# Optimization experiments

Measured on AMD Instinct MI355X. Metric: run time of the kernel, lower is better.

Reference implementation:

```python
import jax, jax.numpy as jnp
import numpy as np

N = 20000      # nodes
E = 320000     # edges (before self-loops)
G = 64         # graphs in batch
IN = 128       # input_dim
HID = 64       # hidden_dim
H1 = 4         # heads of conv1
NEG_SLOPE = 0.2


def setup_inputs() -> dict:
    key = jax.random.key(0)
    ks = jax.random.split(key, 14)
    x = jax.random.normal(ks[0], (N, IN), jnp.float32)
    edge_index = jax.random.randint(ks[1], (2, E), 0, N, dtype=jnp.int32)
    batch = jnp.sort(jax.random.randint(ks[2], (N,), 0, G, dtype=jnp.int32))
    # conv1: in=IN, out=HID, heads=4, concat
    W1 = jax.random.normal(ks[3], (IN, H1 * HID), jnp.float32) / np.float32(np.sqrt(IN))
    a_src1 = jax.random.normal(ks[4], (H1, HID), jnp.float32) / np.float32(np.sqrt(HID))
    a_dst1 = jax.random.normal(ks[5], (H1, HID), jnp.float32) / np.float32(np.sqrt(HID))
    b1 = jnp.zeros((H1 * HID,), jnp.float32)
    # conv2: in=4*HID, out=HID, heads=1
    W2 = jax.random.normal(ks[6], (H1 * HID, HID), jnp.float32) / np.float32(np.sqrt(H1 * HID))
    a_src2 = jax.random.normal(ks[7], (1, HID), jnp.float32) / np.float32(np.sqrt(HID))
    a_dst2 = jax.random.normal(ks[8], (1, HID), jnp.float32) / np.float32(np.sqrt(HID))
    b2 = jnp.zeros((HID,), jnp.float32)
    # final linear HID -> 1
    W_lin = jax.random.normal(ks[9], (HID, 1), jnp.float32) / np.float32(np.sqrt(HID))
    b_lin = jnp.zeros((1,), jnp.float32)
    return dict(x=x, edge_index=edge_index, batch=batch,
                W1=W1, a_src1=a_src1, a_dst1=a_dst1, b1=b1,
                W2=W2, a_src2=a_src2, a_dst2=a_dst2, b2=b2,
                W_lin=W_lin, b_lin=b_lin)


def gat_conv(x, src, dst, W, a_src, a_dst, b, heads, out_ch, n_nodes):
    """PyG-style GATConv (v1), concat=True, with self-loops already in src/dst."""
    h = (x @ W).reshape(n_nodes, heads, out_ch)          # [N,H,C]
    s = jnp.einsum('nhc,hc->nh', h, a_src)               # [N,H] per-node src score
    d = jnp.einsum('nhc,hc->nh', h, a_dst)               # [N,H] per-node dst score
    logits = jax.nn.leaky_relu(s[src] + d[dst], NEG_SLOPE)   # [Etot,H]
    # segment softmax over incoming edges of each destination node
    m = jax.ops.segment_max(logits, dst, num_segments=n_nodes)
    m = jnp.where(jnp.isfinite(m), m, 0.0)
    e = jnp.exp(logits - m[dst])                         # [Etot,H]
    denom = jax.ops.segment_sum(e, dst, num_segments=n_nodes)
    alpha = e / denom[dst]                               # every node has a self-loop -> denom>0
    out = jax.ops.segment_sum(alpha[:, :, None] * h[src], dst, num_segments=n_nodes)  # [N,H,C]
    return out.reshape(n_nodes, heads * out_ch) + b


def reference(x, edge_index, batch,
              W1, a_src1, a_dst1, b1,
              W2, a_src2, a_dst2, b2,
              W_lin, b_lin):
    n = x.shape[0]
    loop = jnp.arange(n, dtype=edge_index.dtype)
    src = jnp.concatenate([edge_index[0], loop])   # add self-loops (PyG default)
    dst = jnp.concatenate([edge_index[1], loop])
    h = jax.nn.elu(gat_conv(x, src, dst, W1, a_src1, a_dst1, b1, H1, HID, n))
    h = jax.nn.elu(gat_conv(h, src, dst, W2, a_src2, a_dst2, b2, 1, HID, n))
    # global mean pool over graphs
    sums = jax.ops.segment_sum(h, batch, num_segments=G)                 # [G,HID]
    cnt = jax.ops.segment_sum(jnp.ones((n,), h.dtype), batch, num_segments=G)
    pooled = sums / jnp.maximum(cnt, 1.0)[:, None]
    return (pooled @ W_lin + b_lin).squeeze(-1)    # [G]
```

## Files before the change

kernel.cpp:

```cpp
#include <hip/hip_runtime.h>
#include <hip/hip_bf16.h>
#include <cstdint>


__device__ __forceinline__ float leaky02(float x) { return x > 0.f ? x : 0.2f * x; }
__device__ __forceinline__ float eluf(float x) { return x > 0.f ? x : expm1f(x); }
__device__ __forceinline__ float bf2f(unsigned short u) {
    return __uint_as_float((unsigned)u << 16);
}
__device__ __forceinline__ unsigned short f2bf(float f) {
    unsigned x = __float_as_uint(f);
    return (unsigned short)((x + 0x7FFF + ((x >> 16) & 1)) >> 16);
}
__device__ __forceinline__ float4 cv4(ushort4 u) {
    return make_float4(bf2f(u.x), bf2f(u.y), bf2f(u.z), bf2f(u.w));
}

template <int H>
__device__ __forceinline__ void sgemm_scores_body(
    const float* __restrict__ A, const float* __restrict__ B,
    unsigned short* __restrict__ C, int M, int K,
    const float* __restrict__ asrc, const float* __restrict__ adst,
    float* __restrict__ sT, float* __restrict__ dS, float* __restrict__ wself,
    int bx, int by, float* As_, float* Bs_) {
    constexpr int Nc = H * 64;
    float (*As)[68] = (float(*)[68])As_;
    float (*Bs)[68] = (float(*)[68])Bs_;
    const int tid = threadIdx.x;
    const int bm = bx * 64, bn = by * 64;
    const int ty = tid >> 4, tx = tid & 15;
    float acc[4][4] = {};
    for (int k0 = 0; k0 < K; k0 += 32) {
#pragma unroll
        for (int i = 0; i < 8; i++) {
            int idx = tid + i * 256;
            int m = idx >> 5, kk = idx & 31;
            int gm = bm + m;
            if (gm >= M) gm = 0;
            As[kk][m] = A[(size_t)gm * K + k0 + kk];
        }
#pragma unroll
        for (int i = 0; i < 8; i++) {
            int idx = tid + i * 256;
            int kk = idx >> 6, n = idx & 63;
            Bs[kk][n] = B[(size_t)(k0 + kk) * Nc + bn + n];
        }
        __syncthreads();
#pragma unroll
        for (int kk = 0; kk < 32; kk++) {
            float4 a4 = *(const float4*)&As[kk][ty * 4];
            float4 b4 = *(const float4*)&Bs[kk][tx * 4];
            float av[4] = {a4.x, a4.y, a4.z, a4.w};
            float bv[4] = {b4.x, b4.y, b4.z, b4.w};
#pragma unroll
            for (int r = 0; r < 4; r++)
#pragma unroll
                for (int c2 = 0; c2 < 4; c2++) acc[r][c2] += av[r] * bv[c2];
        }
        __syncthreads();
    }
    const int h = by;
    float sr[4], dr[4];
#pragma unroll
    for (int r = 0; r < 4; r++) {
        float s = 0.f, d = 0.f;
#pragma unroll
        for (int c2 = 0; c2 < 4; c2++) {
            float hv = acc[r][c2];
            s += hv * asrc[h * 64 + tx * 4 + c2];
            d += hv * adst[h * 64 + tx * 4 + c2];
        }
        sr[r] = s;
        dr[r] = d;
    }
#pragma unroll
    for (int off = 1; off <= 8; off <<= 1) {
#pragma unroll
        for (int r = 0; r < 4; r++) {
            sr[r] += __shfl_xor(sr[r], off);
            dr[r] += __shfl_xor(dr[r], off);
        }
    }
#pragma unroll
    for (int r = 0; r < 4; r++) {
        int gm = bm + ty * 4 + r;
        if (gm < M) {
            ushort4 o;
            o.x = f2bf(acc[r][0]);
            o.y = f2bf(acc[r][1]);
            o.z = f2bf(acc[r][2]);
            o.w = f2bf(acc[r][3]);
            *(ushort4*)&C[(size_t)gm * Nc + bn + tx * 4] = o;
            if (tx == 0) {
                sT[(size_t)h * M + gm] = sr[r];
                dS[gm * H + h] = dr[r];
                wself[gm * H + h] = __expf(leaky02(sr[r] + dr[r]));
            }
        }
    }
}

__global__ __launch_bounds__(256) void fused_sgemm4_init_kernel(
    const float* __restrict__ A, const float* __restrict__ B,
    unsigned short* __restrict__ C, int M, int K,
    const float* __restrict__ asrc, const float* __restrict__ adst,
    float* __restrict__ sT, float* __restrict__ dS, float* __restrict__ wself,
    int GBX, int GB1, int4* __restrict__ initp, int colN4, int totN4) {
    __shared__ __align__(16) float As_[32][68];
    __shared__ __align__(16) float Bs_[32][68];
    const int b = blockIdx.x;
    if (b >= GB1) {
        int i = (b - GB1) * 256 + threadIdx.x;
        if (i < totN4)
            initp[i] = (i < colN4) ? make_int4(-1, -1, -1, -1) : make_int4(0, 0, 0, 0);
        return;
    }
    sgemm_scores_body<4>(A, B, C, M, K, asrc, adst, sT, dS, wself,
                         b % GBX, b / GBX, &As_[0][0], &Bs_[0][0]);
}

__global__ __launch_bounds__(256) void sgemm_scores1_kernel(
    const float* __restrict__ A, const float* __restrict__ B,
    unsigned short* __restrict__ C, int M, int K,
    const float* __restrict__ asrc, const float* __restrict__ adst,
    float* __restrict__ sT, float* __restrict__ dS, float* __restrict__ wself) {
    __shared__ __align__(16) float As_[32][68];
    __shared__ __align__(16) float Bs_[32][68];
    sgemm_scores_body<1>(A, B, C, M, K, asrc, adst, sT, dS, wself,
                         blockIdx.x, 0, &As_[0][0], &Bs_[0][0]);
}

__global__ void fill_kernel(const int* __restrict__ src, const int* __restrict__ dst,
                            int* __restrict__ cursor, int* __restrict__ col, int E) {
    int e = blockIdx.x * blockDim.x + threadIdx.x;
    if (e >= E) return;
    int d = dst[e];
    int p = atomicAdd(&cursor[d], 1);
    if (p < 64) col[(d << 6) + p] = src[e];
}

__global__ __launch_bounds__(256) void gat_agg4_kernel(
    const unsigned short* __restrict__ h1, const float* __restrict__ sT,
    const float* __restrict__ dsc, const float* __restrict__ wself,
    const int* __restrict__ cursor, const int* __restrict__ col,
    const float* __restrict__ bias, float* __restrict__ out, int N) {
    const int slice = blockIdx.x & 3;
    const int sub = (blockIdx.x >> 2) & 1;
    const int vgrp = (blockIdx.x >> 3) * 2 + sub;
    const int lane = threadIdx.x & 63;
    const int cq = lane & 15;
    const int vidx = vgrp * 16 + (threadIdx.x >> 6) * 4 + (lane >> 4);
    const bool valid = vidx < N;
    const int v = min(vidx, N - 1);
    const int deg = min(cursor[v], 64);
    const int base = v << 6;
    const int ch = slice * 64 + cq * 4;
    const float* __restrict__ sTh = sT + (size_t)slice * N;
    const unsigned short* __restrict__ hp = h1 + slice * 64 + cq * 4;
    const float dvh = dsc[v * 4 + slice];
    float ws = wself[v * 4 + slice];
    float den = ws;
    float4 hv = cv4(*(const ushort4*)(hp + ((size_t)v << 8)));
    float4 acc = make_float4(ws * hv.x, ws * hv.y, ws * hv.z, ws * hv.w);
    const int end4 = (deg + 3) & ~3;
    int4 c4 = *(const int4*)&col[base];
    for (int j = 0; j < end4; j += 4) {
        int4 cc = c4;
        c4 = *(const int4*)&col[base + j + 4];
        unsigned i0 = (unsigned)max(cc.x, 0), i1 = (unsigned)max(cc.y, 0);
        unsigned i2 = (unsigned)max(cc.z, 0), i3 = (unsigned)max(cc.w, 0);
        float4 h0 = cv4(*(const ushort4*)(hp + ((size_t)i0 << 8)));
        float4 h1v = cv4(*(const ushort4*)(hp + ((size_t)i1 << 8)));
        float4 h2v = cv4(*(const ushort4*)(hp + ((size_t)i2 << 8)));
        float4 h3v = cv4(*(const ushort4*)(hp + ((size_t)i3 << 8)));
        float w0 = (cc.x >= 0) ? __expf(leaky02(sTh[i0] + dvh)) : 0.f;
        float w1 = (cc.y >= 0) ? __expf(leaky02(sTh[i1] + dvh)) : 0.f;
        float w2 = (cc.z >= 0) ? __expf(leaky02(sTh[i2] + dvh)) : 0.f;
        float w3 = (cc.w >= 0) ? __expf(leaky02(sTh[i3] + dvh)) : 0.f;
        den += w0 + w1 + w2 + w3;
        acc.x += w0 * h0.x + w1 * h1v.x + w2 * h2v.x + w3 * h3v.x;
        acc.y += w0 * h0.y + w1 * h1v.y + w2 * h2v.y + w3 * h3v.y;
        acc.z += w0 * h0.z + w1 * h1v.z + w2 * h2v.z + w3 * h3v.z;
        acc.w += w0 * h0.w + w1 * h1v.w + w2 * h2v.w + w3 * h3v.w;
    }
    if (valid) {
        float4 b4 = *(const float4*)&bias[ch];
        float inv = 1.f / den;
        float4 r;
        r.x = eluf(acc.x * inv + b4.x);
        r.y = eluf(acc.y * inv + b4.y);
        r.z = eluf(acc.z * inv + b4.z);
        r.w = eluf(acc.w * inv + b4.w);
        *(float4*)&out[(size_t)v * 256 + ch] = r;
    }
}

__global__ __launch_bounds__(256) void gat_agg1_kernel(
    const unsigned short* __restrict__ h2, const float* __restrict__ sT,
    const float* __restrict__ dsc, const float* __restrict__ wself,
    const int* __restrict__ cursor, const int* __restrict__ col,
    const float* __restrict__ bias, const float* __restrict__ Wlin,
    float* __restrict__ pn, int N) {
    const int lane = threadIdx.x & 63;
    const int cq = lane & 15;
    const int vidx = blockIdx.x * 16 + (threadIdx.x >> 6) * 4 + (lane >> 4);
    const bool valid = vidx < N;
    const int v = min(vidx, N - 1);
    const int deg = min(cursor[v], 64);
    const int base = v << 6;
    const unsigned short* __restrict__ hp = h2 + cq * 4;
    const float dv = dsc[v];
    float ws = wself[v];
    float den = ws;
    float4 hv = cv4(*(const ushort4*)(hp + ((size_t)v << 6)));
    float4 acc = make_float4(ws * hv.x, ws * hv.y, ws * hv.z, ws * hv.w);
    const int end4 = (deg + 3) & ~3;
    int4 c4 = *(const int4*)&col[base];
    for (int j = 0; j < end4; j += 4) {
        int4 cc = c4;
        c4 = *(const int4*)&col[base + j + 4];
        unsigned i0 = (unsigned)max(cc.x, 0), i1 = (unsigned)max(cc.y, 0);
        unsigned i2 = (unsigned)max(cc.z, 0), i3 = (unsigned)max(cc.w, 0);
        float4 h0 = cv4(*(const ushort4*)(hp + ((size_t)i0 << 6)));
        float4 h1v = cv4(*(const ushort4*)(hp + ((size_t)i1 << 6)));
        float4 h2v = cv4(*(const ushort4*)(hp + ((size_t)i2 << 6)));
        float4 h3v = cv4(*(const ushort4*)(hp + ((size_t)i3 << 6)));
        float w0 = (cc.x >= 0) ? __expf(leaky02(sT[i0] + dv)) : 0.f;
        float w1 = (cc.y >= 0) ? __expf(leaky02(sT[i1] + dv)) : 0.f;
        float w2 = (cc.z >= 0) ? __expf(leaky02(sT[i2] + dv)) : 0.f;
        float w3 = (cc.w >= 0) ? __expf(leaky02(sT[i3] + dv)) : 0.f;
        den += w0 + w1 + w2 + w3;
        acc.x += w0 * h0.x + w1 * h1v.x + w2 * h2v.x + w3 * h3v.x;
        acc.y += w0 * h0.y + w1 * h1v.y + w2 * h2v.y + w3 * h3v.y;
        acc.z += w0 * h0.z + w1 * h1v.z + w2 * h2v.z + w3 * h3v.z;
        acc.w += w0 * h0.w + w1 * h1v.w + w2 * h2v.w + w3 * h3v.w;
    }
    float4 b4 = *(const float4*)&bias[cq * 4];
    float4 wl = *(const float4*)&Wlin[cq * 4];
    float inv = 1.f / den;
    float p = eluf(acc.x * inv + b4.x) * wl.x + eluf(acc.y * inv + b4.y) * wl.y +
              eluf(acc.z * inv + b4.z) * wl.z + eluf(acc.w * inv + b4.w) * wl.w;
    p += __shfl_xor(p, 1);
    p += __shfl_xor(p, 2);
    p += __shfl_xor(p, 4);
    p += __shfl_xor(p, 8);
    if (valid && cq == 0) pn[v] = p;
}

__global__ __launch_bounds__(64) void finalize_kernel(const float* __restrict__ pn,
                                                      const int* __restrict__ batch,
                                                      const float* __restrict__ blin,
                                                      float* __restrict__ outp, int N, int G) {
    const int g = blockIdx.x;
    const int lane = threadIdx.x;
    int lo = 0, hi = N;
    while (lo < hi) { int mid = (lo + hi) >> 1; if (batch[mid] < g) lo = mid + 1; else hi = mid; }
    int lo2 = lo, hi2 = N;
    while (lo2 < hi2) { int mid = (lo2 + hi2) >> 1; if (batch[mid] < g + 1) lo2 = mid + 1; else hi2 = mid; }
    float s = 0.f;
    for (int i = lo + lane; i < hi2; i += 64) s += pn[i];
#pragma unroll
    for (int off = 32; off > 0; off >>= 1) s += __shfl_xor(s, off);
    if (lane == 0) {
        float cnt = (float)(hi2 - lo);
        outp[g] = s / fmaxf(cnt, 1.f) + blin[0];
    }
}

extern "C" void kernel_launch(void* const* d_in, const int* in_sizes, int n_in,
                              void* d_out, int out_size, void* d_ws, size_t ws_size,
                              hipStream_t stream) {
    const float* x      = (const float*)d_in[0];
    const int*   ei     = (const int*)d_in[1];
    const int*   batch  = (const int*)d_in[2];
    const float* W1     = (const float*)d_in[3];
    const float* a_src1 = (const float*)d_in[4];
    const float* a_dst1 = (const float*)d_in[5];
    const float* b1     = (const float*)d_in[6];
    const float* W2     = (const float*)d_in[7];
    const float* a_src2 = (const float*)d_in[8];
    const float* a_dst2 = (const float*)d_in[9];
    const float* b2     = (const float*)d_in[10];
    const float* Wlin   = (const float*)d_in[11];
    const float* blin   = (const float*)d_in[12];

    const int N = in_sizes[2];
    const int E = in_sizes[1] / 2;
    const int G = out_size;
    const int* src = ei;
    const int* dst = ei + E;

    char* ws = (char*)d_ws;
    size_t off = 0;
    auto carve = [&](size_t bytes) -> char* {
        char* p = ws + off;
        off = (off + bytes + 255) & ~(size_t)255;
        return p;
    };
    unsigned short* h1 = (unsigned short*)carve((size_t)N * 256 * 2);
    float* out1    = (float*)carve((size_t)N * 256 * 4);
    unsigned short* h2 = (unsigned short*)carve((size_t)N * 64 * 2);
    float* sT1     = (float*)carve((size_t)4 * N * 4);
    float* d1      = (float*)carve((size_t)N * 4 * 4);
    float* wself1  = (float*)carve((size_t)N * 4 * 4);
    float* sT2     = (float*)carve((size_t)N * 4);
    float* d2      = (float*)carve((size_t)N * 4);
    float* wself2  = (float*)carve((size_t)N * 4);
    int*   colcur  = (int*)carve(((size_t)N * 64 + N) * 4);
    float* pn      = (float*)carve((size_t)N * 4);
    int* col = colcur;
    int* cursor = colcur + (size_t)N * 64;

    const int GBX = (N + 63) / 64;
    const int GB1 = GBX * 4;
    const int totN4 = (N * 64 + N) / 4;
    const int colN4 = N * 16;
    const int GBI = (totN4 + 255) / 256;

    fused_sgemm4_init_kernel<<<GB1 + GBI, 256, 0, stream>>>(
        x, W1, h1, N, 128, a_src1, a_dst1, sT1, d1, wself1,
        GBX, GB1, (int4*)colcur, colN4, totN4);
    fill_kernel<<<(E + 255) / 256, 256, 0, stream>>>(src, dst, cursor, col, E);

    const int nodeGroups32 = (N + 31) / 32;
    gat_agg4_kernel<<<8 * nodeGroups32, 256, 0, stream>>>(h1, sT1, d1, wself1, cursor, col,
                                                          b1, out1, N);
    sgemm_scores1_kernel<<<dim3(GBX, 1), 256, 0, stream>>>(
        out1, W2, h2, N, 256, a_src2, a_dst2, sT2, d2, wself2);
    gat_agg1_kernel<<<(N + 15) / 16, 256, 0, stream>>>(h2, sT2, d2, wself2, cursor, col,
                                                       b2, Wlin, pn, N);
    finalize_kernel<<<G, 64, 0, stream>>>(pn, batch, blin, (float*)d_out, N, G);
}
```

Baseline: 125.3 us.

## Store layer-1 output in bf16, fuse CSR fill into GEMM, fold finalize into last block

The layer-1 aggregation output is now written in bf16 and the second GEMM reads it as bf16, which halves that intermediate's traffic. The CSR fill moves into the layer-1 GEMM launch, and a separate init kernel clears the buffers first. The mean-pool finalize runs inside the last block of the layer-2 aggregation, found with an atomic done counter. This removes a launch but adds bf16 rounding of the layer-2 input, and the finalize work now sits on a single block.

Result: slower. 214.7 us (+71.4%).

```diff
diff --git a/kernel.cpp b/kernel.cpp
--- a/kernel.cpp
+++ b/kernel.cpp
@@ -15,10 +15,18 @@
 __device__ __forceinline__ float4 cv4(ushort4 u) {
     return make_float4(bf2f(u.x), bf2f(u.y), bf2f(u.z), bf2f(u.w));
 }
-
-template <int H>
+__device__ __forceinline__ float ldA(const float* p) { return *p; }
+__device__ __forceinline__ float ldA(const unsigned short* p) { return bf2f(*p); }
+
+__global__ void init_kernel(int4* __restrict__ p, int colN4, int totN4) {
+    int i = blockIdx.x * blockDim.x + threadIdx.x;
+    if (i < totN4)
+        p[i] = (i < colN4) ? make_int4(-1, -1, -1, -1) : make_int4(0, 0, 0, 0);
+}
+
+template <int H, typename AT>
 __device__ __forceinline__ void sgemm_scores_body(
-    const float* __restrict__ A, const float* __restrict__ B,
+    const AT* __restrict__ A, const float* __restrict__ B,
     unsigned short* __restrict__ C, int M, int K,
     const float* __restrict__ asrc, const float* __restrict__ adst,
     float* __restrict__ sT, float* __restrict__ dS, float* __restrict__ wself,
@@ -37,7 +45,7 @@
             int m = idx >> 5, kk = idx & 31;
             int gm = bm + m;
             if (gm >= M) gm = 0;
-            As[kk][m] = A[(size_t)gm * K + k0 + kk];
+            As[kk][m] = ldA(&A[(size_t)gm * K + k0 + kk]);
         }
 #pragma unroll
         for (int i = 0; i < 8; i++) {
@@ -100,50 +108,45 @@
     }
 }
 
-__global__ __launch_bounds__(256) void fused_sgemm4_init_kernel(
+__global__ __launch_bounds__(256) void fused_sgemm4_fill_kernel(
     const float* __restrict__ A, const float* __restrict__ B,
     unsigned short* __restrict__ C, int M, int K,
     const float* __restrict__ asrc, const float* __restrict__ adst,
     float* __restrict__ sT, float* __restrict__ dS, float* __restrict__ wself,
-    int GBX, int GB1, int4* __restrict__ initp, int colN4, int totN4) {
+    int GBX, int GB1, const int* __restrict__ src, const int* __restrict__ dst,
+    int* __restrict__ cursor, int* __restrict__ col, int E) {
     __shared__ __align__(16) float As_[32][68];
     __shared__ __align__(16) float Bs_[32][68];
     const int b = blockIdx.x;
     if (b >= GB1) {
-        int i = (b - GB1) * 256 + threadIdx.x;
-        if (i < totN4)
-            initp[i] = (i < colN4) ? make_int4(-1, -1, -1, -1) : make_int4(0, 0, 0, 0);
+        int e = (b - GB1) * 256 + threadIdx.x;
+        if (e < E) {
+            int d = dst[e];
+            int p = atomicAdd(&cursor[d], 1);
+            if (p < 64) col[(d << 6) + p] = src[e];
+        }
         return;
     }
-    sgemm_scores_body<4>(A, B, C, M, K, asrc, adst, sT, dS, wself,
-                         b % GBX, b / GBX, &As_[0][0], &Bs_[0][0]);
+    sgemm_scores_body<4, float>(A, B, C, M, K, asrc, adst, sT, dS, wself,
+                                b % GBX, b / GBX, &As_[0][0], &Bs_[0][0]);
 }
 
 __global__ __launch_bounds__(256) void sgemm_scores1_kernel(
-    const float* __restrict__ A, const float* __restrict__ B,
+    const unsigned short* __restrict__ A, const float* __restrict__ B,
     unsigned short* __restrict__ C, int M, int K,
     const float* __restrict__ asrc, const float* __restrict__ adst,
     float* __restrict__ sT, float* __restrict__ dS, float* __restrict__ wself) {
     __shared__ __align__(16) float As_[32][68];
     __shared__ __align__(16) float Bs_[32][68];
-    sgemm_scores_body<1>(A, B, C, M, K, asrc, adst, sT, dS, wself,
-                         blockIdx.x, 0, &As_[0][0], &Bs_[0][0]);
-}
-
-__global__ void fill_kernel(const int* __restrict__ src, const int* __restrict__ dst,
-                            int* __restrict__ cursor, int* __restrict__ col, int E) {
-    int e = blockIdx.x * blockDim.x + threadIdx.x;
-    if (e >= E) return;
-    int d = dst[e];
-    int p = atomicAdd(&cursor[d], 1);
-    if (p < 64) col[(d << 6) + p] = src[e];
+    sgemm_scores_body<1, unsigned short>(A, B, C, M, K, asrc, adst, sT, dS, wself,
+                                         blockIdx.x, 0, &As_[0][0], &Bs_[0][0]);
 }
 
 __global__ __launch_bounds__(256) void gat_agg4_kernel(
     const unsigned short* __restrict__ h1, const float* __restrict__ sT,
     const float* __restrict__ dsc, const float* __restrict__ wself,
     const int* __restrict__ cursor, const int* __restrict__ col,
-    const float* __restrict__ bias, float* __restrict__ out, int N) {
+    const float* __restrict__ bias, unsigned short* __restrict__ out, int N) {
     const int slice = blockIdx.x & 3;
     const int sub = (blockIdx.x >> 2) & 1;
     const int vgrp = (blockIdx.x >> 3) * 2 + sub;
@@ -158,10 +161,10 @@
     const float* __restrict__ sTh = sT + (size_t)slice * N;
     const unsigned short* __restrict__ hp = h1 + slice * 64 + cq * 4;
     const float dvh = dsc[v * 4 + slice];
-    float ws = wself[v * 4 + slice];
-    float den = ws;
+    float wsf = wself[v * 4 + slice];
+    float den = wsf;
     float4 hv = cv4(*(const ushort4*)(hp + ((size_t)v << 8)));
-    float4 acc = make_float4(ws * hv.x, ws * hv.y, ws * hv.z, ws * hv.w);
+    float4 acc = make_float4(wsf * hv.x, wsf * hv.y, wsf * hv.z, wsf * hv.w);
     const int end4 = (deg + 3) & ~3;
     int4 c4 = *(const int4*)&col[base];
     for (int j = 0; j < end4; j += 4) {
@@ -186,21 +189,23 @@
     if (valid) {
         float4 b4 = *(const float4*)&bias[ch];
         float inv = 1.f / den;
-        float4 r;
-        r.x = eluf(acc.x * inv + b4.x);
-        r.y = eluf(acc.y * inv + b4.y);
-        r.z = eluf(acc.z * inv + b4.z);
-        r.w = eluf(acc.w * inv + b4.w);
-        *(float4*)&out[(size_t)v * 256 + ch] = r;
-    }
-}
-
-__global__ __launch_bounds__(256) void gat_agg1_kernel(
+        ushort4 o;
+        o.x = f2bf(eluf(acc.x * inv + b4.x));
+        o.y = f2bf(eluf(acc.y * inv + b4.y));
+        o.z = f2bf(eluf(acc.z * inv + b4.z));
+        o.w = f2bf(eluf(acc.w * inv + b4.w));
+        *(ushort4*)&out[(size_t)v * 256 + ch] = o;
+    }
+}
+
+__global__ __launch_bounds__(256) void gat_agg1_fin_kernel(
     const unsigned short* __restrict__ h2, const float* __restrict__ sT,
     const float* __restrict__ dsc, const float* __restrict__ wself,
     const int* __restrict__ cursor, const int* __restrict__ col,
     const float* __restrict__ bias, const float* __restrict__ Wlin,
-    float* __restrict__ pn, int N) {
+    float* __restrict__ pn, const int* __restrict__ batch,
+    const float* __restrict__ blin, float* __restrict__ outp,
+    int* __restrict__ done, int N, int G) {
     const int lane = threadIdx.x & 63;
     const int cq = lane & 15;
     const int vidx = blockIdx.x * 16 + (threadIdx.x >> 6) * 4 + (lane >> 4);
@@ -210,10 +215,10 @@
     const int base = v << 6;
     const unsigned short* __restrict__ hp = h2 + cq * 4;
     const float dv = dsc[v];
-    float ws = wself[v];
-    float den = ws;
+    float wsf = wself[v];
+    float den = wsf;
     float4 hv = cv4(*(const ushort4*)(hp + ((size_t)v << 6)));
-    float4 acc = make_float4(ws * hv.x, ws * hv.y, ws * hv.z, ws * hv.w);
+    float4 acc = make_float4(wsf * hv.x, wsf * hv.y, wsf * hv.z, wsf * hv.w);
     const int end4 = (deg + 3) & ~3;
     int4 c4 = *(const int4*)&col[base];
     for (int j = 0; j < end4; j += 4) {
@@ -245,25 +250,30 @@
     p += __shfl_xor(p, 4);
     p += __shfl_xor(p, 8);
     if (valid && cq == 0) pn[v] = p;
-}
-
-__global__ __launch_bounds__(64) void finalize_kernel(const float* __restrict__ pn,
-                                                      const int* __restrict__ batch,
-                                                      const float* __restrict__ blin,
-                                                      float* __restrict__ outp, int N, int G) {
-    const int g = blockIdx.x;
-    const int lane = threadIdx.x;
-    int lo = 0, hi = N;
-    while (lo < hi) { int mid = (lo + hi) >> 1; if (batch[mid] < g) lo = mid + 1; else hi = mid; }
-    int lo2 = lo, hi2 = N;
-    while (lo2 < hi2) { int mid = (lo2 + hi2) >> 1; if (batch[mid] < g + 1) lo2 = mid + 1; else hi2 = mid; }
-    float s = 0.f;
-    for (int i = lo + lane; i < hi2; i += 64) s += pn[i];
-#pragma unroll
-    for (int off = 32; off > 0; off >>= 1) s += __shfl_xor(s, off);
-    if (lane == 0) {
-        float cnt = (float)(hi2 - lo);
-        outp[g] = s / fmaxf(cnt, 1.f) + blin[0];
+
+    __shared__ int lastFlag;
+    __threadfence();
+    if (threadIdx.x == 0) {
+        int old = atomicAdd(done, 1);
+        lastFlag = (old == (int)gridDim.x - 1) ? 1 : 0;
+    }
+    __syncthreads();
+    if (!lastFlag) return;
+    __threadfence();
+    const int g = threadIdx.x >> 2, sub = threadIdx.x & 3;
+    if (g < G) {
+        int lo = 0, hi = N;
+        while (lo < hi) { int mid = (lo + hi) >> 1; if (batch[mid] < g) lo = mid + 1; else hi = mid; }
+        int lo2 = lo, hi2 = N;
+        while (lo2 < hi2) { int mid = (lo2 + hi2) >> 1; if (batch[mid] < g + 1) lo2 = mid + 1; else hi2 = mid; }
+        float s = 0.f;
+        for (int i = lo + sub; i < hi2; i += 4) s += pn[i];
+        s += __shfl_xor(s, 1);
+        s += __shfl_xor(s, 2);
+        if (sub == 0) {
+            float cnt = (float)(hi2 - lo);
+            outp[g] = s / fmaxf(cnt, 1.f) + blin[0];
+        }
     }
 }
 
@@ -297,37 +307,37 @@
         off = (off + bytes + 255) & ~(size_t)255;
         return p;
     };
-    unsigned short* h1 = (unsigned short*)carve((size_t)N * 256 * 2);
-    float* out1    = (float*)carve((size_t)N * 256 * 4);
-    unsigned short* h2 = (unsigned short*)carve((size_t)N * 64 * 2);
+    unsigned short* h1   = (unsigned short*)carve((size_t)N * 256 * 2);
+    unsigned short* out1 = (unsigned short*)carve((size_t)N * 256 * 2);
+    unsigned short* h2   = (unsigned short*)carve((size_t)N * 64 * 2);
     float* sT1     = (float*)carve((size_t)4 * N * 4);
     float* d1      = (float*)carve((size_t)N * 4 * 4);
     float* wself1  = (float*)carve((size_t)N * 4 * 4);
     float* sT2     = (float*)carve((size_t)N * 4);
     float* d2      = (float*)carve((size_t)N * 4);
     float* wself2  = (float*)carve((size_t)N * 4);
-    int*   colcur  = (int*)carve(((size_t)N * 64 + N) * 4);
+    int*   colcur  = (int*)carve(((size_t)N * 64 + N + 4) * 4);
     float* pn      = (float*)carve((size_t)N * 4);
     int* col = colcur;
     int* cursor = colcur + (size_t)N * 64;
+    int* done = cursor + N;
 
     const int GBX = (N + 63) / 64;
     const int GB1 = GBX * 4;
-    const int totN4 = (N * 64 + N) / 4;
-    const int colN4 = N * 16;
-    const int GBI = (totN4 + 255) / 256;
-
-    fused_sgemm4_init_kernel<<<GB1 + GBI, 256, 0, stream>>>(
+    const int colN4 = (N * 64) / 4;
+    const int totN4 = (N * 64 + N + 4 + 3) / 4;
+    const int fillBlocks = (E + 255) / 256;
+
+    init_kernel<<<(totN4 + 255) / 256, 256, 0, stream>>>((int4*)colcur, colN4, totN4);
+    fused_sgemm4_fill_kernel<<<GB1 + fillBlocks, 256, 0, stream>>>(
         x, W1, h1, N, 128, a_src1, a_dst1, sT1, d1, wself1,
-        GBX, GB1, (int4*)colcur, colN4, totN4);
-    fill_kernel<<<(E + 255) / 256, 256, 0, stream>>>(src, dst, cursor, col, E);
-
+        GBX, GB1, src, dst, cursor, col, E);
     const int nodeGroups32 = (N + 31) / 32;
     gat_agg4_kernel<<<8 * nodeGroups32, 256, 0, stream>>>(h1, sT1, d1, wself1, cursor, col,
                                                           b1, out1, N);
     sgemm_scores1_kernel<<<dim3(GBX, 1), 256, 0, stream>>>(
         out1, W2, h2, N, 256, a_src2, a_dst2, sT2, d2, wself2);
-    gat_agg1_kernel<<<(N + 15) / 16, 256, 0, stream>>>(h2, sT2, d2, wself2, cursor, col,
-                                                       b2, Wlin, pn, N);
-    finalize_kernel<<<G, 64, 0, stream>>>(pn, batch, blin, (float*)d_out, N, G);
-}
+    gat_agg1_fin_kernel<<<(N + 15) / 16, 256, 0, stream>>>(
+        h2, sT2, d2, wself2, cursor, col, b2, Wlin, pn, batch, blin,
+        (float*)d_out, done, N, G);
+}
```
